# Kernel optimization log

Hardware: AMD Instinct MI355X
Metric: run time of the kernel (lower is better)

Reference implementation:

```python
import jax, jax.numpy as jnp
import numpy as np
import math

DIM = 512
HEADS = 8
DHEAD = DIM // HEADS            # 64
NB_FEATURES = int(DHEAD * math.log(DHEAD))  # 266
B, N = 2, 2048
CHUNK = 128                     # chunk size for the causal scan
EPS = 1e-4


def gaussian_orthogonal_random_matrix(nb_rows, nb_cols, rng):
    # blocks of orthogonal rows (Q^T of QR of a gaussian), scaled by chi-distributed norms
    blocks = []
    n_full = nb_rows // nb_cols
    for _ in range(n_full):
        q, _ = np.linalg.qr(rng.standard_normal((nb_cols, nb_cols)))
        blocks.append(q.T)
    rem = nb_rows - n_full * nb_cols
    if rem > 0:
        q, _ = np.linalg.qr(rng.standard_normal((nb_cols, nb_cols)))
        blocks.append(q.T[:rem])
    mat = np.concatenate(blocks, axis=0)
    multiplier = np.linalg.norm(rng.standard_normal((nb_rows, nb_cols)), axis=1)
    return (multiplier[:, None] * mat).astype(np.float32)


def setup_inputs() -> dict:
    key = jax.random.key(0)
    k1, k2, k3 = jax.random.split(key, 3)
    rng = np.random.default_rng(0)
    x = jax.random.normal(k1, (B, N, DIM), dtype=jnp.float32)
    w_qkv = jax.random.normal(k2, (DIM, 3 * DIM), dtype=jnp.float32) / math.sqrt(DIM)
    w_out = jax.random.normal(k3, (DIM, DIM), dtype=jnp.float32) / math.sqrt(DIM)
    b_out = jnp.zeros((DIM,), dtype=jnp.float32)
    proj = jnp.asarray(gaussian_orthogonal_random_matrix(NB_FEATURES, DHEAD, rng))
    return {"x": x, "w_qkv": w_qkv, "w_out": w_out, "b_out": b_out, "proj": proj}


def softmax_kernel(data, proj, is_query):
    # data: [b,h,n,d], proj: [m,d]
    d = data.shape[-1]
    data_normalizer = d ** -0.25
    ratio = proj.shape[0] ** -0.5
    data_dash = jnp.einsum('bhnd,md->bhnm', data_normalizer * data, proj)
    diag_data = jnp.sum(data * data, axis=-1, keepdims=True) * 0.5 * (data_normalizer ** 2)
    if is_query:
        stab = jnp.max(data_dash, axis=-1, keepdims=True)
    else:
        stab = jnp.max(data_dash)
    return ratio * (jnp.exp(data_dash - diag_data - stab) + EPS)


def causal_linear_attention(q, k, v, chunk=CHUNK):
    # q,k: [b,h,n,m]; v: [b,h,n,d]
    # out_n = sum_m q_nm * (sum_{i<=n} k_im v_i) / (sum_{i<=n} k_im)   (per-feature normalization,
    # identical to causal_linear_attention_noncuda), computed in chunks for memory efficiency.
    b, h, n, m = q.shape
    d = v.shape[-1]
    nc = n // chunk
    qc = jnp.moveaxis(q.reshape(b, h, nc, chunk, m), 2, 0)  # [nc,b,h,C,m]
    kc = jnp.moveaxis(k.reshape(b, h, nc, chunk, m), 2, 0)
    vc = jnp.moveaxis(v.reshape(b, h, nc, chunk, d), 2, 0)

    def step(carry, inp):
        kv_state, ksum_state = carry            # [b,h,m,d], [b,h,m]
        qch, kch, vch = inp                     # [b,h,C,m], [b,h,C,m], [b,h,C,d]
        ksum = ksum_state[:, :, None, :] + jnp.cumsum(kch, axis=2)          # [b,h,C,m]
        ctx = kv_state[:, :, None, :, :] + jnp.cumsum(
            jnp.einsum('bhcm,bhcd->bhcmd', kch, vch), axis=2)               # [b,h,C,m,d]
        out = jnp.einsum('bhcm,bhcmd->bhcd', qch, ctx / ksum[..., None])
        return (ctx[:, :, -1], ksum[:, :, -1]), out

    init = (jnp.zeros((b, h, m, d), q.dtype), jnp.zeros((b, h, m), q.dtype))
    _, outs = jax.lax.scan(step, init, (qc, kc, vc))
    return jnp.moveaxis(outs, 0, 2).reshape(b, h, n, d)


def reference(x, w_qkv, w_out, b_out, proj):
    b, n, _ = x.shape
    qkv = x @ w_qkv                                   # [b,n,3*dim]
    q, k, v = jnp.split(qkv, 3, axis=-1)
    split = lambda t: t.reshape(b, n, HEADS, DHEAD).transpose(0, 2, 1, 3)  # b h n d
    q, k, v = split(q), split(k), split(v)
    qp = softmax_kernel(q, proj, is_query=True)       # [b,h,n,m]
    kp = softmax_kernel(k, proj, is_query=False)
    out = causal_linear_attention(qp, kp, v)          # [b,h,n,d]
    out = out.transpose(0, 2, 1, 3).reshape(b, n, DIM)
    return out @ w_out + b_out
```

## Files before the change

### kernel.cpp

```cpp
#include <hip/hip_runtime.h>
#include <math.h>

#define DIMX 512
#define NHEADS 8
#define DH 64
#define MF 266
#define MP 272
#define MPS 288
#define NB 2
#define NSEQ 2048
#define NROWS (NB*NSEQ)
#define NBH 16
#define CHK 64
#define NCH 32
#define EPSF 1e-4f
#define LDT 40
#define LDP 72

typedef __attribute__((ext_vector_type(8))) short short8;
typedef __attribute__((ext_vector_type(4))) float f32x4;
typedef unsigned short ushort_t;

__device__ __forceinline__ unsigned fkey(float f){
    unsigned u = __float_as_uint(f);
    return (f < 0.0f) ? ~u : (u | 0x80000000u);
}
__device__ __forceinline__ float fdec(unsigned k){
    unsigned u = (k & 0x80000000u) ? (k & 0x7fffffffu) : ~k;
    return __uint_as_float(u);
}
__device__ __forceinline__ float b2f(ushort_t u){
    return __uint_as_float(((unsigned)u) << 16);
}

__device__ __forceinline__ void bsplit(float a, ushort_t& h, ushort_t& l){
    unsigned u = __float_as_uint(a);
    unsigned r = (u + 0x7fffu + ((u >> 16) & 1u)) & 0xffff0000u;
    h = (ushort_t)(r >> 16);
    float res = a - __uint_as_float(r);
    unsigned v = __float_as_uint(res);
    unsigned r2 = v + 0x7fffu + ((v >> 16) & 1u);
    l = (ushort_t)(r2 >> 16);
}

__global__ __launch_bounds__(256) void split_kernel(
    const float* __restrict__ A, ushort_t* __restrict__ H, ushort_t* __restrict__ L, int total4)
{
    int i = blockIdx.x * 256 + threadIdx.x;
    if (i >= total4) return;
    float4 f = ((const float4*)A)[i];
    ushort_t h0,h1,h2,h3,l0,l1,l2,l3;
    bsplit(f.x,h0,l0); bsplit(f.y,h1,l1); bsplit(f.z,h2,l2); bsplit(f.w,h3,l3);
    ((ushort4*)H)[i] = make_ushort4(h0,h1,h2,h3);
    ((ushort4*)L)[i] = make_ushort4(l0,l1,l2,l3);
}

__global__ __launch_bounds__(256) void splitT_kernel(
    const float* __restrict__ W, ushort_t* __restrict__ Th, ushort_t* __restrict__ Tl,
    int K, int N)
{
    __shared__ ushort_t Sh[64][72], Sl[64][72];
    const int k0 = blockIdx.y * 64, n0 = blockIdx.x * 64;
    const int tid = threadIdx.x;
    {
        const int kk = tid >> 4, nq = (tid & 15) * 4;
        for (int p = 0; p < 4; p++) {
            int k = p*16 + kk;
            float4 f = *(const float4*)&W[(size_t)(k0 + k)*N + n0 + nq];
            ushort_t h, l;
            bsplit(f.x,h,l); Sh[nq+0][k]=h; Sl[nq+0][k]=l;
            bsplit(f.y,h,l); Sh[nq+1][k]=h; Sl[nq+1][k]=l;
            bsplit(f.z,h,l); Sh[nq+2][k]=h; Sl[nq+2][k]=l;
            bsplit(f.w,h,l); Sh[nq+3][k]=h; Sl[nq+3][k]=l;
        }
    }
    __syncthreads();
    {
        const int n = tid >> 2, ks = (tid & 3) * 16;
        for (int q = 0; q < 2; q++) {
            uint4 vh = *(const uint4*)&Sh[n][ks + q*8];
            uint4 vl = *(const uint4*)&Sl[n][ks + q*8];
            *(uint4*)&Th[(size_t)(n0 + n)*K + k0 + ks + q*8] = vh;
            *(uint4*)&Tl[(size_t)(n0 + n)*K + k0 + ks + q*8] = vl;
        }
    }
}

__global__ __launch_bounds__(256) void gemm_bf16s(
    const ushort_t* __restrict__ Ah, const ushort_t* __restrict__ Al,
    const ushort_t* __restrict__ Bh, const ushort_t* __restrict__ Bl,
    const float* __restrict__ bias, float* __restrict__ C,
    int M, int N, int K)
{
    __shared__ ushort_t sAh[128*LDT], sAl[128*LDT], sBh[128*LDT], sBl[128*LDT];
    const int tid = threadIdx.x;
    const int m0 = blockIdx.y * 128, n0 = blockIdx.x * 128;
    const int lane = tid & 63, w = tid >> 6;
    const int wr = w >> 1, wc = w & 1;
    const int lr = lane & 15;
    const int lsu = (lane >> 4) * 8;
    const int r = tid >> 1, sg = (tid & 1) * 16;
    const size_t gA = (size_t)(m0 + r)*K + sg;
    const size_t gB = (size_t)(n0 + r)*K + sg;

    f32x4 acc[4][4];
    #pragma unroll
    for (int i=0;i<4;i++)
        #pragma unroll
        for (int j=0;j<4;j++) acc[i][j] = (f32x4){0.f,0.f,0.f,0.f};

    for (int k0 = 0; k0 < K; k0 += 32) {
        uint4 a0 = *(const uint4*)&Ah[gA + k0];
        uint4 a1 = *(const uint4*)&Ah[gA + k0 + 8];
        uint4 a2 = *(const uint4*)&Al[gA + k0];
        uint4 a3 = *(const uint4*)&Al[gA + k0 + 8];
        uint4 b0 = *(const uint4*)&Bh[gB + k0];
        uint4 b1 = *(const uint4*)&Bh[gB + k0 + 8];
        uint4 b2 = *(const uint4*)&Bl[gB + k0];
        uint4 b3 = *(const uint4*)&Bl[gB + k0 + 8];
        __syncthreads();
        *(uint4*)&sAh[r*LDT + sg]     = a0;
        *(uint4*)&sAh[r*LDT + sg + 8] = a1;
        *(uint4*)&sAl[r*LDT + sg]     = a2;
        *(uint4*)&sAl[r*LDT + sg + 8] = a3;
        *(uint4*)&sBh[r*LDT + sg]     = b0;
        *(uint4*)&sBh[r*LDT + sg + 8] = b1;
        *(uint4*)&sBl[r*LDT + sg]     = b2;
        *(uint4*)&sBl[r*LDT + sg + 8] = b3;
        __syncthreads();
        short8 afh[4], afl[4], bfh[4], bfl[4];
        #pragma unroll
        for (int f = 0; f < 4; f++) {
            int ra = (wr*64 + f*16 + lr)*LDT + lsu;
            int rb = (wc*64 + f*16 + lr)*LDT + lsu;
            afh[f] = *(const short8*)&sAh[ra];
            afl[f] = *(const short8*)&sAl[ra];
            bfh[f] = *(const short8*)&sBh[rb];
            bfl[f] = *(const short8*)&sBl[rb];
        }
        #pragma unroll
        for (int i = 0; i < 4; i++)
            #pragma unroll
            for (int j = 0; j < 4; j++) {
                acc[i][j] = __builtin_amdgcn_mfma_f32_16x16x32_bf16(afh[i], bfh[j], acc[i][j], 0, 0, 0);
                acc[i][j] = __builtin_amdgcn_mfma_f32_16x16x32_bf16(afh[i], bfl[j], acc[i][j], 0, 0, 0);
                acc[i][j] = __builtin_amdgcn_mfma_f32_16x16x32_bf16(afl[i], bfh[j], acc[i][j], 0, 0, 0);
            }
    }
    const int crow = (lane >> 4) * 4, ccol = lane & 15;
    #pragma unroll
    for (int i = 0; i < 4; i++) {
        #pragma unroll
        for (int j = 0; j < 4; j++) {
            int col = n0 + wc*64 + j*16 + ccol;
            float bb = bias ? bias[col] : 0.f;
            #pragma unroll
            for (int rr = 0; rr < 4; rr++) {
                int row = m0 + wr*64 + i*16 + crow + rr;
                C[(size_t)row*N + col] = acc[i][j][rr] + bb;
            }
        }
    }
}

template<bool IS_Q>
__global__ __launch_bounds__(256) void feat_kernel(
    const float* __restrict__ qkv, const float* __restrict__ proj,
    float* __restrict__ dashout, ushort_t* __restrict__ oh, ushort_t* __restrict__ ol,
    float* __restrict__ diag_out, unsigned* __restrict__ gmax,
    int coff, float nrm, float ratio)
{
    __shared__ float As[64][68];
    __shared__ float Bs[16][MP+1];
    const int tid = threadIdx.x;
    const int tx = tid & 15, ty = tid >> 4;
    const int bh = blockIdx.y, b = bh >> 3, h = bh & 7;
    const int n0 = blockIdx.x * 64;
    {
        const int r = tid & 63, lq = tid >> 6;
        const float* src = &qkv[(size_t)(b*NSEQ + n0 + r)*(3*DIMX) + coff + h*DH];
        #pragma unroll
        for (int qq = 0; qq < 4; qq++) {
            int c = lq*16 + qq*4;
            float4 f = *(const float4*)&src[c];
            As[c+0][r]=f.x; As[c+1][r]=f.y; As[c+2][r]=f.z; As[c+3][r]=f.w;
        }
    }
    float dash[4][17];
    #pragma unroll
    for (int i=0;i<4;i++)
        #pragma unroll
        for (int j=0;j<17;j++) dash[i][j] = 0.f;
    float dsq[4] = {0.f,0.f,0.f,0.f};
    for (int s = 0; s < 4; s++) {
        __syncthreads();
        for (int idx = tid; idx < MP*4; idx += 256) {
            int m = idx >> 2, qq = idx & 3;
            float4 f = make_float4(0.f,0.f,0.f,0.f);
            if (m < MF) f = *(const float4*)&proj[m*DH + s*16 + qq*4];
            Bs[qq*4+0][m]=f.x; Bs[qq*4+1][m]=f.y; Bs[qq*4+2][m]=f.z; Bs[qq*4+3][m]=f.w;
        }
        __syncthreads();
        #pragma unroll
        for (int kk = 0; kk < 16; kk++) {
            float4 a = *(const float4*)&As[s*16+kk][ty*4];
            float ar[4] = {a.x,a.y,a.z,a.w};
            #pragma unroll
            for (int i=0;i<4;i++) dsq[i] = fmaf(ar[i], ar[i], dsq[i]);
            #pragma unroll
            for (int jj = 0; jj < 17; jj++) {
                float bv = Bs[kk][tx + 16*jj];
                #pragma unroll
                for (int i=0;i<4;i++) dash[i][jj] = fmaf(ar[i], bv, dash[i][jj]);
            }
        }
    }
    const size_t rbase = (size_t)bh*NSEQ + n0 + ty*4;
    if (IS_Q) {
        #pragma unroll
        for (int i=0;i<4;i++){
            float diag = 0.0625f * dsq[i];
            float mx = -1e30f;
            #pragma unroll
            for (int jj=0;jj<17;jj++){
                dash[i][jj] *= nrm;
                if (tx + 16*jj < MF) mx = fmaxf(mx, dash[i][jj]);
            }
            #pragma unroll
            for (int o=1;o<16;o<<=1) mx = fmaxf(mx, __shfl_xor(mx, o, 64));
            ushort_t* orh = &oh[(rbase + i)*MPS];
            ushort_t* orl = &ol[(rbase + i)*MPS];
            #pragma unroll
            for (int jj=0;jj<17;jj++){
                int m = tx + 16*jj;
                float v = (m < MF) ? ratio*(expf(dash[i][jj] - diag - mx) + EPSF) : 0.f;
                ushort_t hh2, ll2;
                bsplit(v, hh2, ll2);
                orh[m] = hh2; orl[m] = ll2;
            }
        }
    } else {
        float wmax = -1e30f;
        #pragma unroll
        for (int i=0;i<4;i++){
            float diag = 0.0625f * dsq[i];
            if (tx == 0) diag_out[rbase + i] = diag;
            float* orow = &dashout[(rbase + i)*MP];
            #pragma unroll
            for (int jj=0;jj<17;jj++){
                float d = dash[i][jj] * nrm;
                int m = tx + 16*jj;
                orow[m] = d;
                if (m < MF) wmax = fmaxf(wmax, d);
            }
        }
        #pragma unroll
        for (int o=1;o<64;o<<=1) wmax = fmaxf(wmax, __shfl_xor(wmax, o, 64));
        if ((tid & 63) == 0) atomicMax(gmax, fkey(wmax));
    }
}

__global__ __launch_bounds__(256) void kexp_kernel(
    const float* __restrict__ dash, const float* __restrict__ diagk,
    const unsigned* __restrict__ gmax,
    ushort_t* __restrict__ kph, ushort_t* __restrict__ kpl, float ratio)
{
    unsigned gid = blockIdx.x * 256u + threadIdx.x;
    if (gid >= (unsigned)NBH*NSEQ*(MPS/4)) return;
    unsigned row = gid / (MPS/4);
    int mq = (int)(gid % (MPS/4)) * 4;
    ushort4 h4 = make_ushort4(0,0,0,0), l4 = make_ushort4(0,0,0,0);
    if (mq < MP) {
        const float stab = fdec(*gmax);
        float dg = diagk[row];
        float4 v = *(const float4*)&dash[(size_t)row*MP + mq];
        float r[4] = {v.x,v.y,v.z,v.w};
        ushort_t hh[4], ll[4];
        #pragma unroll
        for (int j = 0; j < 4; j++) {
            float kv = (mq + j < MF) ? ratio * (expf(r[j] - dg - stab) + EPSF) : 0.f;
            bsplit(kv, hh[j], ll[j]);
        }
        h4 = make_ushort4(hh[0],hh[1],hh[2],hh[3]);
        l4 = make_ushort4(ll[0],ll[1],ll[2],ll[3]);
    }
    *(ushort4*)&kph[(size_t)row*MPS + mq] = h4;
    *(ushort4*)&kpl[(size_t)row*MPS + mq] = l4;
}

__global__ __launch_bounds__(320) void chunk_sums_kernel(
    const ushort_t* __restrict__ kph, const ushort_t* __restrict__ kpl,
    const float* __restrict__ qkv,
    float* __restrict__ ckvT, float* __restrict__ cksum)
{
    __shared__ float vs[CHK][DH];
    const int tid = threadIdx.x;
    const int c = blockIdx.x, bh = blockIdx.y, b = bh >> 3, h = bh & 7;
    for (int idx = tid; idx < CHK*16; idx += 320) {
        int i = idx >> 4, q = idx & 15;
        *(float4*)&vs[i][q*4] =
            *(const float4*)&qkv[(size_t)(b*NSEQ + c*CHK + i)*(3*DIMX) + 2*DIMX + h*DH + q*4];
    }
    __syncthreads();
    if (tid >= 272) return;
    const int mg = tid % 68, dg = tid / 68;
    float acc[4][16] = {};
    float ks[4] = {0.f,0.f,0.f,0.f};
    const size_t kbase = (size_t)(bh*NSEQ + c*CHK)*MPS + mg*4;
    for (int i = 0; i < CHK; i++) {
        ushort4 kh = *(const ushort4*)&kph[kbase + (size_t)i*MPS];
        ushort4 kl = *(const ushort4*)&kpl[kbase + (size_t)i*MPS];
        float kr[4] = {b2f(kh.x)+b2f(kl.x), b2f(kh.y)+b2f(kl.y),
                       b2f(kh.z)+b2f(kl.z), b2f(kh.w)+b2f(kl.w)};
        if (dg == 0) { ks[0]+=kr[0]; ks[1]+=kr[1]; ks[2]+=kr[2]; ks[3]+=kr[3]; }
        #pragma unroll
        for (int t = 0; t < 4; t++) {
            float4 vv = *(const float4*)&vs[i][dg*16 + t*4];
            float vr[4] = {vv.x,vv.y,vv.z,vv.w};
            #pragma unroll
            for (int mi=0;mi<4;mi++){
                acc[mi][t*4+0] = fmaf(kr[mi], vr[0], acc[mi][t*4+0]);
                acc[mi][t*4+1] = fmaf(kr[mi], vr[1], acc[mi][t*4+1]);
                acc[mi][t*4+2] = fmaf(kr[mi], vr[2], acc[mi][t*4+2]);
                acc[mi][t*4+3] = fmaf(kr[mi], vr[3], acc[mi][t*4+3]);
            }
        }
    }
    const size_t tbase = (size_t)(bh*NCH + c)*64;
    #pragma unroll
    for (int dd = 0; dd < 16; dd++) {
        int d = dg*16 + dd;
        *(float4*)&ckvT[(tbase + d)*MP + mg*4] =
            make_float4(acc[0][dd], acc[1][dd], acc[2][dd], acc[3][dd]);
    }
    if (dg == 0) {
        #pragma unroll
        for (int mi=0;mi<4;mi++)
            cksum[(size_t)(bh*NCH + c)*MP + mg*4 + mi] = ks[mi];
    }
}

__global__ __launch_bounds__(256) void prefix_ckvT_kernel(
    const float* __restrict__ ckvT, ushort_t* __restrict__ cth, ushort_t* __restrict__ ctl)
{
    const int bh = blockIdx.y;
    const int dm = blockIdx.x * 256 + threadIdx.x;
    if (dm >= 64*MPS) return;
    const int d = dm / MPS, m = dm % MPS;
    if (m < MP) {
        float run = 0.f;
        #pragma unroll
        for (int c = 0; c < NCH; c++) {
            size_t row = (size_t)(bh*NCH + c)*64 + d;
            ushort_t h, l;
            bsplit(run, h, l);
            cth[row*MPS + m] = h; ctl[row*MPS + m] = l;
            run += ckvT[row*MP + m];
        }
    } else {
        #pragma unroll
        for (int c = 0; c < NCH; c++) {
            size_t row = (size_t)(bh*NCH + c)*64 + d;
            cth[row*MPS + m] = 0; ctl[row*MPS + m] = 0;
        }
    }
}

__global__ __launch_bounds__(320) void prefix_ksum_kernel(float* __restrict__ cksum)
{
    const int bh = blockIdx.x;
    const int m = threadIdx.x;
    if (m >= MP) return;
    float run = 0.f;
    #pragma unroll
    for (int c = 0; c < NCH; c++) {
        size_t idx = (size_t)(bh*NCH + c)*MP + m;
        float v = cksum[idx];
        cksum[idx] = run;
        run += v;
    }
}

__global__ __launch_bounds__(320) void qprime_kernel(
    ushort_t* __restrict__ qph, ushort_t* __restrict__ qpl,
    const ushort_t* __restrict__ kph, const ushort_t* __restrict__ kpl,
    const float* __restrict__ cksum)
{
    const int c = blockIdx.x, bh = blockIdx.y;
    const int m = threadIdx.x;
    if (m >= MPS) return;
    size_t base = (size_t)(bh*NSEQ + c*CHK)*MPS + m;
    if (m < MF) {
        float run = cksum[(size_t)(bh*NCH + c)*MP + m];
        for (int i = 0; i < CHK; i++) {
            size_t idx = base + (size_t)i*MPS;
            run += b2f(kph[idx]) + b2f(kpl[idx]);
            float q = b2f(qph[idx]) + b2f(qpl[idx]);
            q /= run;
            ushort_t h, l;
            bsplit(q, h, l);
            qph[idx] = h; qpl[idx] = l;
        }
    } else {
        for (int i = 0; i < CHK; i++) {
            size_t idx = base + (size_t)i*MPS;
            qph[idx] = 0; qpl[idx] = 0;
        }
    }
}

__global__ __launch_bounds__(256) void attn_mfma(
    const ushort_t* __restrict__ qph, const ushort_t* __restrict__ qpl,
    const ushort_t* __restrict__ kph, const ushort_t* __restrict__ kpl,
    const ushort_t* __restrict__ cth, const ushort_t* __restrict__ ctl,
    const float* __restrict__ qkv,
    ushort_t* __restrict__ aout_h, ushort_t* __restrict__ aout_l)
{
    __shared__ ushort_t tQh[64*LDT], tQl[64*LDT];
    __shared__ ushort_t tKh[64*LDT], tKl[64*LDT];
    __shared__ ushort_t tSh[64*LDT], tSl[64*LDT];
    __shared__ ushort_t VTh[64*LDP], VTl[64*LDP];
    __shared__ ushort_t Ph[64*LDP],  Pl[64*LDP];
    const int tid = threadIdx.x;
    const int c = blockIdx.x, bh = blockIdx.y, b = bh >> 3, hh = bh & 7;
    const size_t rowg = (size_t)bh*NSEQ + c*CHK;
    const size_t rowx = (size_t)b*NSEQ + c*CHK;
    const size_t sbase = (size_t)(bh*NCH + c)*64;

    {
        const int j = tid >> 2, dq = (tid & 3) * 16;
        const float* vsrc = &qkv[(rowx + j)*(3*DIMX) + 2*DIMX + hh*DH + dq];
        #pragma unroll
        for (int p = 0; p < 4; p++) {
            float4 f = *(const float4*)&vsrc[p*4];
            float vr[4] = {f.x,f.y,f.z,f.w};
            #pragma unroll
            for (int wv = 0; wv < 4; wv++) {
                ushort_t h, l;
                bsplit(vr[wv], h, l);
                VTh[(dq + p*4 + wv)*LDP + j] = h;
                VTl[(dq + p*4 + wv)*LDP + j] = l;
            }
        }
    }

    const int lane = tid & 63, w = tid >> 6;
    const int wr = w >> 1, wc = w & 1;
    const int fr = lane & 15, fk = (lane >> 4) * 8;
    const int srow = tid >> 2, sseg = (tid & 3) * 8;
    f32x4 accP[2][2], accO[2][2];
    #pragma unroll
    for (int i=0;i<2;i++)
        #pragma unroll
        for (int j=0;j<2;j++){ accP[i][j]=(f32x4){0,0,0,0}; accO[i][j]=(f32x4){0,0,0,0}; }

    for (int m0 = 0; m0 < MPS; m0 += 32) {
        uint4 gq_h = *(const uint4*)&qph[(rowg + srow)*MPS + m0 + sseg];
        uint4 gq_l = *(const uint4*)&qpl[(rowg + srow)*MPS + m0 + sseg];
        uint4 gk_h = *(const uint4*)&kph[(rowg + srow)*MPS + m0 + sseg];
        uint4 gk_l = *(const uint4*)&kpl[(rowg + srow)*MPS + m0 + sseg];
        uint4 gs_h = *(const uint4*)&cth[(sbase + srow)*MPS + m0 + sseg];
        uint4 gs_l = *(const uint4*)&ctl[(sbase + srow)*MPS + m0 + sseg];
        __syncthreads();
        *(uint4*)&tQh[srow*LDT + sseg] = gq_h;
        *(uint4*)&tQl[srow*LDT + sseg] = gq_l;
        *(uint4*)&tKh[srow*LDT + sseg] = gk_h;
        *(uint4*)&tKl[srow*LDT + sseg] = gk_l;
        *(uint4*)&tSh[srow*LDT + sseg] = gs_h;
        *(uint4*)&tSl[srow*LDT + sseg] = gs_l;
        __syncthreads();
        short8 aQh[2], aQl[2], bKh[2], bKl[2], bSh[2], bSl[2];
        #pragma unroll
        for (int f = 0; f < 2; f++) {
            int ra = (wr*32 + f*16 + fr)*LDT + fk;
            int rb = (wc*32 + f*16 + fr)*LDT + fk;
            aQh[f] = *(const short8*)&tQh[ra];
            aQl[f] = *(const short8*)&tQl[ra];
            bKh[f] = *(const short8*)&tKh[rb];
            bKl[f] = *(const short8*)&tKl[rb];
            bSh[f] = *(const short8*)&tSh[rb];
            bSl[f] = *(const short8*)&tSl[rb];
        }
        #pragma unroll
        for (int i = 0; i < 2; i++)
            #pragma unroll
            for (int j = 0; j < 2; j++) {
                accP[i][j] = __builtin_amdgcn_mfma_f32_16x16x32_bf16(aQh[i], bKh[j], accP[i][j], 0, 0, 0);
                accP[i][j] = __builtin_amdgcn_mfma_f32_16x16x32_bf16(aQh[i], bKl[j], accP[i][j], 0, 0, 0);
                accP[i][j] = __builtin_amdgcn_mfma_f32_16x16x32_bf16(aQl[i], bKh[j], accP[i][j], 0, 0, 0);
                accO[i][j] = __builtin_amdgcn_mfma_f32_16x16x32_bf16(aQh[i], bSh[j], accO[i][j], 0, 0, 0);
                accO[i][j] = __builtin_amdgcn_mfma_f32_16x16x32_bf16(aQh[i], bSl[j], accO[i][j], 0, 0, 0);
                accO[i][j] = __builtin_amdgcn_mfma_f32_16x16x32_bf16(aQl[i], bSh[j], accO[i][j], 0, 0, 0);
            }
    }

    __syncthreads();
    {
        const int crow = (lane >> 4) * 4, ccol = lane & 15;
        #pragma unroll
        for (int i = 0; i < 2; i++)
            #pragma unroll
            for (int j = 0; j < 2; j++) {
                int colg = wc*32 + j*16 + ccol;
                #pragma unroll
                for (int rr = 0; rr < 4; rr++) {
                    int rowg2 = wr*32 + i*16 + crow + rr;
                    float v = (colg <= rowg2) ? accP[i][j][rr] : 0.f;
                    ushort_t h, l;
                    bsplit(v, h, l);
                    Ph[rowg2*LDP + colg] = h;
                    Pl[rowg2*LDP + colg] = l;
                }
            }
    }
    __syncthreads();

    #pragma unroll
    for (int js = 0; js < 2; js++) {
        short8 aPh[2], aPl[2], bVh[2], bVl[2];
        #pragma unroll
        for (int f = 0; f < 2; f++) {
            int ra = (wr*32 + f*16 + fr)*LDP + js*32 + fk;
            int rb = (wc*32 + f*16 + fr)*LDP + js*32 + fk;
            aPh[f] = *(const short8*)&Ph[ra];
            aPl[f] = *(const short8*)&Pl[ra];
            bVh[f] = *(const short8*)&VTh[rb];
            bVl[f] = *(const short8*)&VTl[rb];
        }
        #pragma unroll
        for (int i = 0; i < 2; i++)
            #pragma unroll
            for (int j = 0; j < 2; j++) {
                accO[i][j] = __builtin_amdgcn_mfma_f32_16x16x32_bf16(aPh[i], bVh[j], accO[i][j], 0, 0, 0);
                accO[i][j] = __builtin_amdgcn_mfma_f32_16x16x32_bf16(aPh[i], bVl[j], accO[i][j], 0, 0, 0);
                accO[i][j] = __builtin_amdgcn_mfma_f32_16x16x32_bf16(aPl[i], bVh[j], accO[i][j], 0, 0, 0);
            }
    }

    {
        const int crow = (lane >> 4) * 4, ccol = lane & 15;
        #pragma unroll
        for (int i = 0; i < 2; i++)
            #pragma unroll
            for (int j = 0; j < 2; j++) {
                int d = wc*32 + j*16 + ccol;
                #pragma unroll
                for (int rr = 0; rr < 4; rr++) {
                    int row = wr*32 + i*16 + crow + rr;
                    size_t o = (rowx + row)*DIMX + hh*DH + d;
                    ushort_t h, l;
                    bsplit(accO[i][j][rr], h, l);
                    aout_h[o] = h; aout_l[o] = l;
                }
            }
    }
}

extern "C" void kernel_launch(void* const* d_in, const int* in_sizes, int n_in,
                              void* d_out, int out_size, void* d_ws, size_t ws_size,
                              hipStream_t stream)
{
    (void)in_sizes; (void)n_in; (void)out_size; (void)ws_size;
    const float* x     = (const float*)d_in[0];
    const float* w_qkv = (const float*)d_in[1];
    const float* w_out = (const float*)d_in[2];
    const float* b_out = (const float*)d_in[3];
    const float* proj  = (const float*)d_in[4];
    float* out = (float*)d_out;

    char* ws = (char*)d_ws;
    size_t off = 0;
    auto alloc = [&](size_t bytes) -> char* {
        char* p = ws + off;
        off += (bytes + 255) & ~(size_t)255;
        return p;
    };
    float* qkv       = (float*)alloc((size_t)NROWS*3*DIMX*sizeof(float));
    float* dash      = (float*)alloc((size_t)NBH*NSEQ*MP*sizeof(float));
    ushort_t* qph    = (ushort_t*)alloc((size_t)NBH*NSEQ*MPS*sizeof(ushort_t));
    ushort_t* qpl    = (ushort_t*)alloc((size_t)NBH*NSEQ*MPS*sizeof(ushort_t));
    ushort_t* kph    = (ushort_t*)alloc((size_t)NBH*NSEQ*MPS*sizeof(ushort_t));
    ushort_t* kpl    = (ushort_t*)alloc((size_t)NBH*NSEQ*MPS*sizeof(ushort_t));
    ushort_t* cth    = (ushort_t*)alloc((size_t)NBH*NCH*64*MPS*sizeof(ushort_t));
    ushort_t* ctl    = (ushort_t*)alloc((size_t)NBH*NCH*64*MPS*sizeof(ushort_t));
    float* cksum     = (float*)alloc((size_t)NBH*NCH*MP*sizeof(float));
    float* diagk     = (float*)alloc((size_t)NBH*NSEQ*sizeof(float));
    unsigned* gmax   = (unsigned*)alloc(256);
    ushort_t* xs_h   = (ushort_t*)alloc((size_t)NROWS*DIMX*sizeof(ushort_t));
    ushort_t* xs_l   = (ushort_t*)alloc((size_t)NROWS*DIMX*sizeof(ushort_t));
    ushort_t* wqt_h  = (ushort_t*)alloc((size_t)(3*DIMX)*DIMX*sizeof(ushort_t));
    ushort_t* wqt_l  = (ushort_t*)alloc((size_t)(3*DIMX)*DIMX*sizeof(ushort_t));
    ushort_t* wot_h  = (ushort_t*)alloc((size_t)DIMX*DIMX*sizeof(ushort_t));
    ushort_t* wot_l  = (ushort_t*)alloc((size_t)DIMX*DIMX*sizeof(ushort_t));
    float* ckvT      = dash;
    ushort_t* aout_h = xs_h;
    ushort_t* aout_l = xs_l;

    const float nrm   = (float)pow(64.0, -0.25);
    const float ratio = (float)(1.0 / sqrt(266.0));

    hipMemsetAsync(gmax, 0, sizeof(unsigned), stream);
    split_kernel<<<dim3((NROWS*DIMX/4 + 255)/256), 256, 0, stream>>>(x, xs_h, xs_l, NROWS*DIMX/4);
    splitT_kernel<<<dim3(3*DIMX/64, DIMX/64), 256, 0, stream>>>(w_qkv, wqt_h, wqt_l, DIMX, 3*DIMX);
    splitT_kernel<<<dim3(DIMX/64, DIMX/64), 256, 0, stream>>>(w_out, wot_h, wot_l, DIMX, DIMX);
    gemm_bf16s<<<dim3(3*DIMX/128, NROWS/128), 256, 0, stream>>>(
        xs_h, xs_l, wqt_h, wqt_l, nullptr, qkv, NROWS, 3*DIMX, DIMX);
    feat_kernel<true ><<<dim3(32, 16), 256, 0, stream>>>(
        qkv, proj, nullptr, qph, qpl, nullptr, nullptr, 0, nrm, ratio);
    feat_kernel<false><<<dim3(32, 16), 256, 0, stream>>>(
        qkv, proj, dash, nullptr, nullptr, diagk, gmax, DIMX, nrm, ratio);
    kexp_kernel<<<dim3((NBH*NSEQ*(MPS/4) + 255)/256), 256, 0, stream>>>(
        dash, diagk, gmax, kph, kpl, ratio);
    chunk_sums_kernel<<<dim3(NCH, NBH), 320, 0, stream>>>(kph, kpl, qkv, ckvT, cksum);
    prefix_ckvT_kernel<<<dim3((64*MPS + 255)/256, NBH), 256, 0, stream>>>(ckvT, cth, ctl);
    prefix_ksum_kernel<<<dim3(NBH), 320, 0, stream>>>(cksum);
    qprime_kernel<<<dim3(NCH, NBH), 320, 0, stream>>>(qph, qpl, kph, kpl, cksum);
    attn_mfma<<<dim3(NCH, NBH), 256, 0, stream>>>(
        qph, qpl, kph, kpl, cth, ctl, qkv, aout_h, aout_l);
    gemm_bf16s<<<dim3(DIMX/128, NROWS/128), 256, 0, stream>>>(
        aout_h, aout_l, wot_h, wot_l, b_out, out, NROWS, DIMX, DIMX);
}
```

Before: 268.8 us.

## Compute random-feature projections with split-bf16 MFMA and store key dash in bf16 pairs

Replaces the scalar FP32 feature-projection kernel with an MFMA version that uses split bf16 (hi/lo, three products) for both data and a pre-split, pre-scaled projection matrix. The key path now writes its pre-exponent dash values as bf16 hi/lo pairs into the kp buffers and then exponentiates in place, instead of going through a separate FP32 dash buffer. The aim is to cut the FP32 ALU cost of the projection and the extra memory traffic of the FP32 intermediate. In exchange it drops the lo*lo term and stores the key dash at reduced precision before the exp, and it adds a small kernel to split the projection matrix.

```diff
diff --git a/kernel.cpp b/kernel.cpp
--- a/kernel.cpp
+++ b/kernel.cpp
@@ -84,6 +84,26 @@
             *(uint4*)&Tl[(size_t)(n0 + n)*K + k0 + ks + q*8] = vl;
         }
     }
+}
+
+__global__ __launch_bounds__(256) void splitP_kernel(
+    const float* __restrict__ proj, ushort_t* __restrict__ ph, ushort_t* __restrict__ pl,
+    float nrm)
+{
+    int idx = blockIdx.x * 256 + threadIdx.x;
+    if (idx >= MPS*64/4) return;
+    int m = idx >> 4, kq = (idx & 15) * 4;
+    ushort4 h4 = make_ushort4(0,0,0,0), l4 = make_ushort4(0,0,0,0);
+    if (m < MF) {
+        float4 f = *(const float4*)&proj[m*64 + kq];
+        ushort_t hh[4], ll[4];
+        bsplit(f.x*nrm,hh[0],ll[0]); bsplit(f.y*nrm,hh[1],ll[1]);
+        bsplit(f.z*nrm,hh[2],ll[2]); bsplit(f.w*nrm,hh[3],ll[3]);
+        h4 = make_ushort4(hh[0],hh[1],hh[2],hh[3]);
+        l4 = make_ushort4(ll[0],ll[1],ll[2],ll[3]);
+    }
+    *(ushort4*)&ph[(size_t)m*64 + kq] = h4;
+    *(ushort4*)&pl[(size_t)m*64 + kq] = l4;
 }
 
 __global__ __launch_bounds__(256) void gemm_bf16s(
@@ -164,128 +184,157 @@
 }
 
 template<bool IS_Q>
-__global__ __launch_bounds__(256) void feat_kernel(
-    const float* __restrict__ qkv, const float* __restrict__ proj,
-    float* __restrict__ dashout, ushort_t* __restrict__ oh, ushort_t* __restrict__ ol,
+__global__ __launch_bounds__(256) void feat_mfma(
+    const float* __restrict__ qkv,
+    const ushort_t* __restrict__ pjh, const ushort_t* __restrict__ pjl,
+    ushort_t* __restrict__ oh, ushort_t* __restrict__ ol,
     float* __restrict__ diag_out, unsigned* __restrict__ gmax,
-    int coff, float nrm, float ratio)
-{
-    __shared__ float As[64][68];
-    __shared__ float Bs[16][MP+1];
+    int coff, float ratio)
+{
+    __shared__ ushort_t sDh[64*LDP], sDl[64*LDP];
+    __shared__ ushort_t sPh[32*LDP], sPl[32*LDP];
+    __shared__ float dsqs[64];
     const int tid = threadIdx.x;
-    const int tx = tid & 15, ty = tid >> 4;
     const int bh = blockIdx.y, b = bh >> 3, h = bh & 7;
     const int n0 = blockIdx.x * 64;
     {
-        const int r = tid & 63, lq = tid >> 6;
-        const float* src = &qkv[(size_t)(b*NSEQ + n0 + r)*(3*DIMX) + coff + h*DH];
-        #pragma unroll
-        for (int qq = 0; qq < 4; qq++) {
-            int c = lq*16 + qq*4;
-            float4 f = *(const float4*)&src[c];
-            As[c+0][r]=f.x; As[c+1][r]=f.y; As[c+2][r]=f.z; As[c+3][r]=f.w;
-        }
-    }
-    float dash[4][17];
-    #pragma unroll
-    for (int i=0;i<4;i++)
-        #pragma unroll
-        for (int j=0;j<17;j++) dash[i][j] = 0.f;
-    float dsq[4] = {0.f,0.f,0.f,0.f};
-    for (int s = 0; s < 4; s++) {
+        const int r = tid >> 2, sgq = (tid & 3) * 16;
+        const float* src = &qkv[(size_t)(b*NSEQ + n0 + r)*(3*DIMX) + coff + h*DH + sgq];
+        float vals[16];
+        float ss = 0.f;
+        #pragma unroll
+        for (int p = 0; p < 4; p++) {
+            float4 f = *(const float4*)&src[p*4];
+            vals[p*4+0]=f.x; vals[p*4+1]=f.y; vals[p*4+2]=f.z; vals[p*4+3]=f.w;
+            ss = fmaf(f.x,f.x, fmaf(f.y,f.y, fmaf(f.z,f.z, fmaf(f.w,f.w, ss))));
+        }
+        ss += __shfl_xor(ss, 1, 64);
+        ss += __shfl_xor(ss, 2, 64);
+        if ((tid & 3) == 0) dsqs[r] = ss;
+        #pragma unroll
+        for (int p = 0; p < 16; p++) {
+            ushort_t hh2, ll2;
+            bsplit(vals[p], hh2, ll2);
+            sDh[r*LDP + sgq + p] = hh2;
+            sDl[r*LDP + sgq + p] = ll2;
+        }
+    }
+    __syncthreads();
+    const int lane = tid & 63, w = tid >> 6;
+    const int fr = lane & 15, fk = (lane >> 4) * 8;
+    short8 aDh[2], aDl[2];
+    #pragma unroll
+    for (int ks = 0; ks < 2; ks++) {
+        int ra = (w*16 + fr)*LDP + ks*32 + fk;
+        aDh[ks] = *(const short8*)&sDh[ra];
+        aDl[ks] = *(const short8*)&sDl[ra];
+    }
+    f32x4 acc[18];
+    #pragma unroll
+    for (int t = 0; t < 18; t++) acc[t] = (f32x4){0.f,0.f,0.f,0.f};
+    #pragma unroll
+    for (int it = 0; it < 9; it++) {
+        const int m0 = it*32;
         __syncthreads();
-        for (int idx = tid; idx < MP*4; idx += 256) {
-            int m = idx >> 2, qq = idx & 3;
-            float4 f = make_float4(0.f,0.f,0.f,0.f);
-            if (m < MF) f = *(const float4*)&proj[m*DH + s*16 + qq*4];
-            Bs[qq*4+0][m]=f.x; Bs[qq*4+1][m]=f.y; Bs[qq*4+2][m]=f.z; Bs[qq*4+3][m]=f.w;
+        {
+            int r2 = tid >> 3, sg2 = (tid & 7) * 8;
+            *(uint4*)&sPh[r2*LDP + sg2] = *(const uint4*)&pjh[(size_t)(m0 + r2)*64 + sg2];
+            *(uint4*)&sPl[r2*LDP + sg2] = *(const uint4*)&pjl[(size_t)(m0 + r2)*64 + sg2];
         }
         __syncthreads();
         #pragma unroll
-        for (int kk = 0; kk < 16; kk++) {
-            float4 a = *(const float4*)&As[s*16+kk][ty*4];
-            float ar[4] = {a.x,a.y,a.z,a.w};
-            #pragma unroll
-            for (int i=0;i<4;i++) dsq[i] = fmaf(ar[i], ar[i], dsq[i]);
-            #pragma unroll
-            for (int jj = 0; jj < 17; jj++) {
-                float bv = Bs[kk][tx + 16*jj];
-                #pragma unroll
-                for (int i=0;i<4;i++) dash[i][jj] = fmaf(ar[i], bv, dash[i][jj]);
-            }
-        }
-    }
-    const size_t rbase = (size_t)bh*NSEQ + n0 + ty*4;
+        for (int mt = 0; mt < 2; mt++) {
+            short8 bh_[2], bl_[2];
+            #pragma unroll
+            for (int ks = 0; ks < 2; ks++) {
+                int rb = (mt*16 + fr)*LDP + ks*32 + fk;
+                bh_[ks] = *(const short8*)&sPh[rb];
+                bl_[ks] = *(const short8*)&sPl[rb];
+            }
+            #pragma unroll
+            for (int ks = 0; ks < 2; ks++) {
+                acc[it*2+mt] = __builtin_amdgcn_mfma_f32_16x16x32_bf16(aDh[ks], bh_[ks], acc[it*2+mt], 0, 0, 0);
+                acc[it*2+mt] = __builtin_amdgcn_mfma_f32_16x16x32_bf16(aDh[ks], bl_[ks], acc[it*2+mt], 0, 0, 0);
+                acc[it*2+mt] = __builtin_amdgcn_mfma_f32_16x16x32_bf16(aDl[ks], bh_[ks], acc[it*2+mt], 0, 0, 0);
+            }
+        }
+    }
+    const size_t rbase = (size_t)bh*NSEQ + n0;
+    const int crow = (lane >> 4) * 4, ccol = lane & 15;
+    const int rw = w*16 + crow;
+    float dg0[4];
+    #pragma unroll
+    for (int rr = 0; rr < 4; rr++) dg0[rr] = 0.0625f * dsqs[rw + rr];
+
     if (IS_Q) {
         #pragma unroll
-        for (int i=0;i<4;i++){
-            float diag = 0.0625f * dsq[i];
+        for (int rr = 0; rr < 4; rr++) {
             float mx = -1e30f;
             #pragma unroll
-            for (int jj=0;jj<17;jj++){
-                dash[i][jj] *= nrm;
-                if (tx + 16*jj < MF) mx = fmaxf(mx, dash[i][jj]);
-            }
-            #pragma unroll
-            for (int o=1;o<16;o<<=1) mx = fmaxf(mx, __shfl_xor(mx, o, 64));
-            ushort_t* orh = &oh[(rbase + i)*MPS];
-            ushort_t* orl = &ol[(rbase + i)*MPS];
-            #pragma unroll
-            for (int jj=0;jj<17;jj++){
-                int m = tx + 16*jj;
-                float v = (m < MF) ? ratio*(expf(dash[i][jj] - diag - mx) + EPSF) : 0.f;
-                ushort_t hh2, ll2;
-                bsplit(v, hh2, ll2);
-                orh[m] = hh2; orl[m] = ll2;
+            for (int t = 0; t < 18; t++) {
+                bool valid = (t < 16) || (t == 16 && ccol < (MF - 256));
+                if (valid) mx = fmaxf(mx, acc[t][rr]);
+            }
+            mx = fmaxf(mx, __shfl_xor(mx, 1, 64));
+            mx = fmaxf(mx, __shfl_xor(mx, 2, 64));
+            mx = fmaxf(mx, __shfl_xor(mx, 4, 64));
+            mx = fmaxf(mx, __shfl_xor(mx, 8, 64));
+            float sub = dg0[rr] + mx;
+            ushort_t* orh = &oh[(rbase + rw + rr)*MPS + ccol];
+            ushort_t* orl = &ol[(rbase + rw + rr)*MPS + ccol];
+            #pragma unroll
+            for (int t = 0; t < 18; t++) {
+                bool valid = (t < 16) || (t == 16 && ccol < (MF - 256));
+                float v = valid ? ratio*(expf(acc[t][rr] - sub) + EPSF) : 0.f;
+                ushort_t hh2, ll2; bsplit(v, hh2, ll2);
+                orh[t*16] = hh2; orl[t*16] = ll2;
             }
         }
     } else {
         float wmax = -1e30f;
         #pragma unroll
-        for (int i=0;i<4;i++){
-            float diag = 0.0625f * dsq[i];
-            if (tx == 0) diag_out[rbase + i] = diag;
-            float* orow = &dashout[(rbase + i)*MP];
-            #pragma unroll
-            for (int jj=0;jj<17;jj++){
-                float d = dash[i][jj] * nrm;
-                int m = tx + 16*jj;
-                orow[m] = d;
-                if (m < MF) wmax = fmaxf(wmax, d);
-            }
-        }
-        #pragma unroll
-        for (int o=1;o<64;o<<=1) wmax = fmaxf(wmax, __shfl_xor(wmax, o, 64));
-        if ((tid & 63) == 0) atomicMax(gmax, fkey(wmax));
+        for (int rr = 0; rr < 4; rr++) {
+            if (ccol == 0) diag_out[rbase + rw + rr] = dg0[rr];
+            ushort_t* orh = &oh[(rbase + rw + rr)*MPS + ccol];
+            ushort_t* orl = &ol[(rbase + rw + rr)*MPS + ccol];
+            #pragma unroll
+            for (int t = 0; t < 18; t++) {
+                float v = acc[t][rr];
+                bool valid = (t < 16) || (t == 16 && ccol < (MF - 256));
+                if (valid) wmax = fmaxf(wmax, v);
+                ushort_t hh2, ll2; bsplit(v, hh2, ll2);
+                orh[t*16] = hh2; orl[t*16] = ll2;
+            }
+        }
+        #pragma unroll
+        for (int o = 1; o < 64; o <<= 1) wmax = fmaxf(wmax, __shfl_xor(wmax, o, 64));
+        if (lane == 0) atomicMax(gmax, fkey(wmax));
     }
 }
 
 __global__ __launch_bounds__(256) void kexp_kernel(
-    const float* __restrict__ dash, const float* __restrict__ diagk,
-    const unsigned* __restrict__ gmax,
-    ushort_t* __restrict__ kph, ushort_t* __restrict__ kpl, float ratio)
+    ushort_t* __restrict__ kph, ushort_t* __restrict__ kpl,
+    const float* __restrict__ diagk, const unsigned* __restrict__ gmax, float ratio)
 {
     unsigned gid = blockIdx.x * 256u + threadIdx.x;
-    if (gid >= (unsigned)NBH*NSEQ*(MPS/4)) return;
+    if (gid >= (unsigned)(NBH*NSEQ*(MPS/4))) return;
     unsigned row = gid / (MPS/4);
     int mq = (int)(gid % (MPS/4)) * 4;
-    ushort4 h4 = make_ushort4(0,0,0,0), l4 = make_ushort4(0,0,0,0);
-    if (mq < MP) {
-        const float stab = fdec(*gmax);
-        float dg = diagk[row];
-        float4 v = *(const float4*)&dash[(size_t)row*MP + mq];
-        float r[4] = {v.x,v.y,v.z,v.w};
-        ushort_t hh[4], ll[4];
-        #pragma unroll
-        for (int j = 0; j < 4; j++) {
-            float kv = (mq + j < MF) ? ratio * (expf(r[j] - dg - stab) + EPSF) : 0.f;
-            bsplit(kv, hh[j], ll[j]);
-        }
-        h4 = make_ushort4(hh[0],hh[1],hh[2],hh[3]);
-        l4 = make_ushort4(ll[0],ll[1],ll[2],ll[3]);
-    }
-    *(ushort4*)&kph[(size_t)row*MPS + mq] = h4;
-    *(ushort4*)&kpl[(size_t)row*MPS + mq] = l4;
+    const float stab = fdec(*gmax);
+    const float dg = diagk[row];
+    size_t idx = (size_t)row*MPS + mq;
+    ushort4 h4 = *(const ushort4*)&kph[idx];
+    ushort4 l4 = *(const ushort4*)&kpl[idx];
+    float dv[4] = {b2f(h4.x)+b2f(l4.x), b2f(h4.y)+b2f(l4.y),
+                   b2f(h4.z)+b2f(l4.z), b2f(h4.w)+b2f(l4.w)};
+    ushort_t hh[4], ll[4];
+    #pragma unroll
+    for (int j = 0; j < 4; j++) {
+        float kv = (mq + j < MF) ? ratio * (expf(dv[j] - dg - stab) + EPSF) : 0.f;
+        bsplit(kv, hh[j], ll[j]);
+    }
+    *(ushort4*)&kph[idx] = make_ushort4(hh[0],hh[1],hh[2],hh[3]);
+    *(ushort4*)&kpl[idx] = make_ushort4(ll[0],ll[1],ll[2],ll[3]);
 }
 
 __global__ __launch_bounds__(320) void chunk_sums_kernel(
@@ -576,7 +625,7 @@
         return p;
     };
     float* qkv       = (float*)alloc((size_t)NROWS*3*DIMX*sizeof(float));
-    float* dash      = (float*)alloc((size_t)NBH*NSEQ*MP*sizeof(float));
+    float* ckvT      = (float*)alloc((size_t)NBH*NCH*64*MP*sizeof(float));
     ushort_t* qph    = (ushort_t*)alloc((size_t)NBH*NSEQ*MPS*sizeof(ushort_t));
     ushort_t* qpl    = (ushort_t*)alloc((size_t)NBH*NSEQ*MPS*sizeof(ushort_t));
     ushort_t* kph    = (ushort_t*)alloc((size_t)NBH*NSEQ*MPS*sizeof(ushort_t));
@@ -592,7 +641,8 @@
     ushort_t* wqt_l  = (ushort_t*)alloc((size_t)(3*DIMX)*DIMX*sizeof(ushort_t));
     ushort_t* wot_h  = (ushort_t*)alloc((size_t)DIMX*DIMX*sizeof(ushort_t));
     ushort_t* wot_l  = (ushort_t*)alloc((size_t)DIMX*DIMX*sizeof(ushort_t));
-    float* ckvT      = dash;
+    ushort_t* pjh    = (ushort_t*)alloc((size_t)MPS*64*sizeof(ushort_t));
+    ushort_t* pjl    = (ushort_t*)alloc((size_t)MPS*64*sizeof(ushort_t));
     ushort_t* aout_h = xs_h;
     ushort_t* aout_l = xs_l;
 
@@ -603,14 +653,15 @@
     split_kernel<<<dim3((NROWS*DIMX/4 + 255)/256), 256, 0, stream>>>(x, xs_h, xs_l, NROWS*DIMX/4);
     splitT_kernel<<<dim3(3*DIMX/64, DIMX/64), 256, 0, stream>>>(w_qkv, wqt_h, wqt_l, DIMX, 3*DIMX);
     splitT_kernel<<<dim3(DIMX/64, DIMX/64), 256, 0, stream>>>(w_out, wot_h, wot_l, DIMX, DIMX);
+    splitP_kernel<<<dim3((MPS*64/4 + 255)/256), 256, 0, stream>>>(proj, pjh, pjl, nrm);
     gemm_bf16s<<<dim3(3*DIMX/128, NROWS/128), 256, 0, stream>>>(
         xs_h, xs_l, wqt_h, wqt_l, nullptr, qkv, NROWS, 3*DIMX, DIMX);
-    feat_kernel<true ><<<dim3(32, 16), 256, 0, stream>>>(
-        qkv, proj, nullptr, qph, qpl, nullptr, nullptr, 0, nrm, ratio);
-    feat_kernel<false><<<dim3(32, 16), 256, 0, stream>>>(
-        qkv, proj, dash, nullptr, nullptr, diagk, gmax, DIMX, nrm, ratio);
+    feat_mfma<true ><<<dim3(32, 16), 256, 0, stream>>>(
+        qkv, pjh, pjl, qph, qpl, nullptr, nullptr, 0, ratio);
+    feat_mfma<false><<<dim3(32, 16), 256, 0, stream>>>(
+        qkv, pjh, pjl, kph, kpl, diagk, gmax, DIMX, ratio);
     kexp_kernel<<<dim3((NBH*NSEQ*(MPS/4) + 255)/256), 256, 0, stream>>>(
-        dash, diagk, gmax, kph, kpl, ratio);
+        kph, kpl, diagk, gmax, ratio);
     chunk_sums_kernel<<<dim3(NCH, NBH), 320, 0, stream>>>(kph, kpl, qkv, ckvT, cksum);
     prefix_ckvT_kernel<<<dim3((64*MPS + 255)/256, NBH), 256, 0, stream>>>(ckvT, cth, ctl);
     prefix_ksum_kernel<<<dim3(NBH), 320, 0, stream>>>(cksum);
```

New measurement: 248.6 us. -7.5%, faster.
